# Performance work log

Hardware: AMD Instinct MI355X
Metric: run time of the kernel (lower is better)

## Reference

```python
import jax, jax.numpy as jnp
import numpy as np

NUM_HEADS = 16

def setup_inputs() -> dict:
    key = jax.random.key(0)
    ks = jax.random.split(key, 8)
    B, S, X, D = 2, 2048, 1, 1024
    scale = 1.0 / np.sqrt(D)
    return {
        "query": jax.random.normal(ks[0], (B, S, X, D), jnp.float32),
        "key": jax.random.normal(ks[1], (B, S, X, D), jnp.float32),
        "value": jax.random.normal(ks[2], (B, S, X, D), jnp.float32),
        "Wq": jax.random.normal(ks[3], (D, D), jnp.float32) * scale,
        "bq": jnp.zeros((D,), jnp.float32),
        "Wk": jax.random.normal(ks[4], (D, D), jnp.float32) * scale,
        "bk": jnp.zeros((D,), jnp.float32),
        "Wv": jax.random.normal(ks[5], (D, D), jnp.float32) * scale,
        "bv": jnp.zeros((D,), jnp.float32),
        "Wo": jax.random.normal(ks[6], (D, D), jnp.float32) * scale,
        "bo": jnp.zeros((D,), jnp.float32),
    }

def _split_heads(x, B, H):
    # [B, S, X, D] -> [B, H, S*X, depth]
    D = x.shape[-1]
    return x.reshape(B, -1, H, D // H).transpose(0, 2, 1, 3)

def reference(query, key, value, Wq, bq, Wk, bk, Wv, bv, Wo, bo):
    B, S, X, D = query.shape
    H = NUM_HEADS
    q = _split_heads(query @ Wq + bq, B, H)   # [B,H,L,dh], L=S*X
    k = _split_heads(key @ Wk + bk, B, H)
    v = _split_heads(value @ Wv + bv, B, H)
    dh = k.shape[-1]
    logits = jnp.einsum("bhqd,bhkd->bhqk", q, k) / jnp.sqrt(jnp.float32(dh))
    attn = jax.nn.softmax(logits, axis=-1)
    out = jnp.einsum("bhqk,bhkd->bhqd", attn, v)   # [B,H,L,dh]
    out = out.transpose(0, 2, 1, 3).reshape(B, S, -1, D)  # [B,S,X,D]
    return out @ Wo + bo
```

## Files before the change

kernel.cpp:

```cpp
#include <hip/hip_runtime.h>
#include <cstdint>
#include <cstddef>

typedef __bf16 bf16x8 __attribute__((ext_vector_type(8)));
typedef float f32x4 __attribute__((ext_vector_type(4)));
typedef float f32x16 __attribute__((ext_vector_type(16)));
typedef unsigned short u16;
typedef unsigned int u32;

static constexpr int Bn = 2;
static constexpr int L  = 2048;
static constexpr int Dm = 1024;
static constexpr int H  = 16;
static constexpr int DH = 64;
static constexpr int M  = Bn * L;
static constexpr size_t PER = (size_t)Bn * H * L * DH;
static constexpr int NQ = Bn * H * L;

#define SC 0.18033688f

__device__ __forceinline__ u16 f2bf(float f) {
    union { float f; u32 u; } v; v.f = f;
    u32 u = v.u + 0x7FFFu + ((v.u >> 16) & 1u);
    return (u16)(u >> 16);
}

__device__ __forceinline__ u32 pk_bf16(float a, float b) {
#if __has_builtin(__builtin_amdgcn_cvt_pk_bf16_f32)
    typedef __bf16 bf16x2_t __attribute__((ext_vector_type(2)));
    bf16x2_t t = __builtin_amdgcn_cvt_pk_bf16_f32(a, b);
    u32 r; __builtin_memcpy(&r, &t, 4); return r;
#else
    return (u32)f2bf(a) | ((u32)f2bf(b) << 16);
#endif
}
__device__ __forceinline__ u16 f2bf1(float f) { return (u16)(pk_bf16(f, f) & 0xffffu); }

__device__ __forceinline__ void gl2lds16(const void* g, void* l) {
    __builtin_amdgcn_global_load_lds(
        (const __attribute__((address_space(1))) u32*)(uintptr_t)g,
        (__attribute__((address_space(3))) u32*)(uintptr_t)l, 16, 0, 0);
}

__global__ __launch_bounds__(256) void convert_in(
    const float* __restrict__ q, const float* __restrict__ k, const float* __restrict__ v,
    u16* __restrict__ dst)
{
    const float* src = (blockIdx.y == 0) ? q : (blockIdx.y == 1) ? k : v;
    u16* d = dst + (size_t)blockIdx.y * M * Dm;
    const size_t t = (size_t)blockIdx.x * 256 + threadIdx.x;
    const float4* s4 = reinterpret_cast<const float4*>(src) + t * 2;
    float4 f0 = s4[0], f1 = s4[1];
    u32 o[4] = { pk_bf16(f0.x, f0.y), pk_bf16(f0.z, f0.w),
                 pk_bf16(f1.x, f1.y), pk_bf16(f1.z, f1.w) };
    reinterpret_cast<uint4*>(d)[t] = *reinterpret_cast<uint4*>(o);
}

__global__ __launch_bounds__(256) void convert_wt(
    const float* __restrict__ Wq, const float* __restrict__ Wk,
    const float* __restrict__ Wv, const float* __restrict__ Wo,
    u16* __restrict__ dst)
{
    __shared__ u16 Ts[64][72];
    const int z = blockIdx.z;
    const float* W = (z == 0) ? Wq : (z == 1) ? Wk : (z == 2) ? Wv : Wo;
    u16* o = dst + (size_t)z * Dm * Dm;
    const int n0 = blockIdx.x * 64, k0 = blockIdx.y * 64;
    const int tid = threadIdx.x;

    {
        const int kr = tid >> 2, nc = (tid & 3) * 16;
        const float* s = W + (size_t)(k0 + kr) * Dm + n0 + nc;
        const float4* s4 = reinterpret_cast<const float4*>(s);
        float4 a = s4[0], b = s4[1], c = s4[2], d = s4[3];
        u32 t[8] = { pk_bf16(a.x, a.y), pk_bf16(a.z, a.w), pk_bf16(b.x, b.y), pk_bf16(b.z, b.w),
                     pk_bf16(c.x, c.y), pk_bf16(c.z, c.w), pk_bf16(d.x, d.y), pk_bf16(d.z, d.w) };
        *reinterpret_cast<uint4*>(&Ts[kr][nc])     = reinterpret_cast<uint4*>(t)[0];
        *reinterpret_cast<uint4*>(&Ts[kr][nc + 8]) = reinterpret_cast<uint4*>(t)[1];
    }
    __syncthreads();
    {
        const int nr = tid >> 2, kc = (tid & 3) * 16;
        u16 w[16];
        #pragma unroll
        for (int j = 0; j < 16; ++j) w[j] = Ts[kc + j][nr];
        u16* dptr = o + (size_t)(n0 + nr) * Dm + k0 + kc;
        *reinterpret_cast<uint4*>(dptr)     = reinterpret_cast<uint4*>(w)[0];
        *reinterpret_cast<uint4*>(dptr + 8) = reinterpret_cast<uint4*>(w)[1];
    }
}

__global__ __launch_bounds__(256) void gemm_qkv(
    const u16* __restrict__ Abuf, const u16* __restrict__ Wtb,
    const float* __restrict__ bq, const float* __restrict__ bk, const float* __restrict__ bv,
    u16* __restrict__ Qh, u16* __restrict__ Kh, u16* __restrict__ Vth)
{
    __shared__ __align__(16) char smem[36864];

    const int tid = threadIdx.x;
    const int wave = tid >> 6, lane = tid & 63;
    const int quad = lane >> 4, l16 = lane & 15;
    const int wr = wave >> 1, wc = wave & 1;
    const int z = blockIdx.z;
    const u16* A  = Abuf + (size_t)z * M * Dm;
    const u16* Bt = Wtb  + (size_t)z * Dm * Dm;
    const float* bias = (z == 0) ? bq : (z == 1) ? bk : bv;
    u16* out = (z == 0) ? Qh : (z == 1) ? Kh : Vth;

    const int bid = blockIdx.y * 8 + blockIdx.x;
    const int m_idx = 4 * (bid & 7) + ((bid >> 3) & 3);
    const int n_idx = bid >> 5;
    const int n0 = n_idx * 128, m0 = m_idx * 128;

    const int srow = lane >> 2;
    const int skc  = (lane & 3) * 8;

    f32x4 acc[4][4] = {};

    auto stage = [&](int k0, int bi) {
        #pragma unroll
        for (int i = 0; i < 2; ++i) {
            const int ra = i * 64 + wave * 16;
            gl2lds16(A  + (size_t)(m0 + ra + srow) * Dm + k0 + skc, smem + bi * 8192 + ra * 64);
            gl2lds16(Bt + (size_t)(n0 + ra + srow) * Dm + k0 + skc, smem + 16384 + bi * 8192 + ra * 64);
        }
    };

    stage(0, 0);
    for (int k0 = 0, it = 0; k0 < Dm; k0 += 32, ++it) {
        const int cb = it & 1;
        __syncthreads();
        if (k0 + 32 < Dm) stage(k0 + 32, cb ^ 1);
        const u16* Asb = (const u16*)(smem + cb * 8192);
        const u16* Bsb = (const u16*)(smem + 16384 + cb * 8192);
        bf16x8 af[4], bf[4];
        #pragma unroll
        for (int t = 0; t < 4; ++t) {
            af[t] = *reinterpret_cast<const bf16x8*>(&Asb[(wr * 64 + t * 16 + l16) * 32 + quad * 8]);
            bf[t] = *reinterpret_cast<const bf16x8*>(&Bsb[(wc * 64 + t * 16 + l16) * 32 + quad * 8]);
        }
        #pragma unroll
        for (int mt = 0; mt < 4; ++mt)
            #pragma unroll
            for (int nt = 0; nt < 4; ++nt)
                acc[mt][nt] = __builtin_amdgcn_mfma_f32_16x16x32_bf16(af[mt], bf[nt], acc[mt][nt], 0, 0, 0);
    }

    __syncthreads();
    u16* tile = (u16*)smem + wave * 4608;
    const float qscale = (z == 0) ? SC : 1.0f;
    #pragma unroll
    for (int nt = 0; nt < 4; ++nt) {
        const int n = n0 + wc * 64 + nt * 16 + l16;
        const float badd = bias[n];
        const int cc = nt * 16 + l16;
        #pragma unroll
        for (int mt = 0; mt < 4; ++mt) {
            #pragma unroll
            for (int r = 0; r < 4; ++r) {
                const int rr = mt * 16 + quad * 4 + r;
                const u16 vv = f2bf1((acc[mt][nt][r] + badd) * qscale);
                if (z == 2) tile[cc * 72 + rr] = vv;
                else        tile[rr * 72 + cc] = vv;
            }
        }
    }
    __syncthreads();

    const int rsub = lane >> 3;
    const int csub = (lane & 7) * 8;
    const int h2 = (n0 + wc * 64) >> 6;
    const int mb = m0 + wr * 64;
    const int bb = mb >> 11, ll0 = mb & 2047;
    if (z == 2) {
        const size_t baseV = ((size_t)(bb * H + h2)) * DH * L;
        #pragma unroll
        for (int j = 0; j < 8; ++j) {
            const int d = j * 8 + rsub;
            uint4 vv = *reinterpret_cast<const uint4*>(&tile[d * 72 + csub]);
            *reinterpret_cast<uint4*>(out + baseV + (size_t)d * L + ll0 + csub) = vv;
        }
    } else {
        const size_t base = ((size_t)(bb * H + h2)) * L * DH;
        #pragma unroll
        for (int j = 0; j < 8; ++j) {
            const int row = j * 8 + rsub;
            uint4 vv = *reinterpret_cast<const uint4*>(&tile[row * 72 + csub]);
            *reinterpret_cast<uint4*>(out + base + (size_t)(ll0 + row) * DH + csub) = vv;
        }
    }
}

__global__ __launch_bounds__(256) void attn(
    const u16* __restrict__ Qh, const u16* __restrict__ Kh,
    const u16* __restrict__ Vth, u16* __restrict__ Opart, float* __restrict__ rsums)
{
    __shared__ __align__(16) char smem[32768];
    u16* Os = (u16*)smem;

    const int tid  = threadIdx.x;
    const int wave = tid >> 6, lane = tid & 63;
    const int l31  = lane & 31, hh = lane >> 5;
    const int qt = blockIdx.x >> 1, half = blockIdx.x & 1;
    const int h = blockIdx.y, b = blockIdx.z;
    const size_t hb = ((size_t)(b * H + h)) * L * DH;
    const int q0 = qt * 128 + wave * 32;

    u16*  Op = Opart + (size_t)half * PER;
    float* rp = rsums + (size_t)half * NQ;

    bf16x8 qf[4];
    {
        const u16* qp = Qh + hb + (size_t)(q0 + l31) * DH + hh * 8;
        #pragma unroll
        for (int c = 0; c < 4; ++c)
            qf[c] = *reinterpret_cast<const bf16x8*>(qp + c * 16);
    }

    bf16x8 ones;
    {
        u32 ov[4] = { 0x3F803F80u, 0x3F803F80u, 0x3F803F80u, 0x3F803F80u };
        ones = *reinterpret_cast<bf16x8*>(ov);
    }

    const int r_off = lane >> 3;
    const int s_sl  = lane & 7;

    auto stage = [&](int kt, int bi) {
        char* base = smem + bi * 16384;
        #pragma unroll
        for (int i = 0; i < 2; ++i) {
            const int rr = wave * 16 + i * 8 + r_off;
            gl2lds16(Kh  + hb + (size_t)(kt * 64 + rr) * DH + ((s_sl ^ (rr & 7)) << 3),
                     base + (wave * 16 + i * 8) * 128);
            gl2lds16(Vth + hb + (size_t)rr * L + kt * 64 + ((s_sl ^ (rr & 7)) << 3),
                     base + 8192 + (wave * 16 + i * 8) * 128);
        }
    };

    int vbK[2], vbV[2];
    #pragma unroll
    for (int t = 0; t < 2; ++t) {
        const int rr = t * 32 + l31;
        vbK[t] = rr * 128 + ((rr & 7) << 4);
        vbV[t] = 8192 + rr * 128 + ((rr & 7) << 4);
    }

    f32x16 oacc[2] = {};
    f32x16 oaccR = {};

    const int kt0 = half * 16;
    stage(kt0, 0);
    for (int ktl = 0; ktl < 16; ++ktl) {
        const int cb = ktl & 1;
        __syncthreads();
        if (ktl + 1 < 16) stage(kt0 + ktl + 1, cb ^ 1);
        const char* ldsb = smem + cb * 16384;

        f32x16 st[2] = {};
        #pragma unroll
        for (int t = 0; t < 2; ++t) {
            #pragma unroll
            for (int c = 0; c < 4; ++c) {
                bf16x8 kf = *reinterpret_cast<const bf16x8*>(ldsb + (vbK[t] ^ (((c << 1) | hh) << 4)));
                st[t] = __builtin_amdgcn_mfma_f32_32x32x16_bf16(kf, qf[c], st[t], 0, 0, 0);
            }
        }

        bf16x8 pfrag[4];
        #pragma unroll
        for (int t = 0; t < 2; ++t) {
            float p[16];
            #pragma unroll
            for (int rr = 0; rr < 16; ++rr)
                p[rr] = __builtin_amdgcn_exp2f(st[t][rr]);
            #pragma unroll
            for (int g = 0; g < 2; ++g) {
                float* pg = p + g * 8;
                u32 w0 = pk_bf16(pg[0], pg[1]);
                u32 w1 = pk_bf16(pg[2], pg[3]);
                u32 w2 = pk_bf16(pg[4], pg[5]);
                u32 w3 = pk_bf16(pg[6], pg[7]);
                asm volatile("v_permlane32_swap_b32 %0, %1" : "+v"(w0), "+v"(w2));
                asm volatile("v_permlane32_swap_b32 %0, %1" : "+v"(w1), "+v"(w3));
                u32 pkv[4] = { w0, w1, w2, w3 };
                pfrag[t * 2 + g] = *reinterpret_cast<bf16x8*>(pkv);
            }
        }

        #pragma unroll
        for (int c = 0; c < 4; ++c) {
            #pragma unroll
            for (int t = 0; t < 2; ++t) {
                bf16x8 vf = *reinterpret_cast<const bf16x8*>(ldsb + (vbV[t] ^ (((c << 1) | hh) << 4)));
                oacc[t] = __builtin_amdgcn_mfma_f32_32x32x16_bf16(vf, pfrag[c], oacc[t], 0, 0, 0);
            }
            oaccR = __builtin_amdgcn_mfma_f32_32x32x16_bf16(ones, pfrag[c], oaccR, 0, 0, 0);
        }
    }

    #pragma unroll
    for (int pass = 0; pass < 2; ++pass) {
        __syncthreads();
        if ((wave >> 1) == pass) {
            const int qloc = (wave & 1) * 32 + l31;
            #pragma unroll
            for (int t = 0; t < 2; ++t) {
                #pragma unroll
                for (int rq = 0; rq < 4; ++rq) {
                    const int d0 = t * 32 + rq * 8 + hh * 4;
                    *reinterpret_cast<u32*>(&Os[qloc * 72 + d0]) =
                        pk_bf16(oacc[t][rq * 4 + 0], oacc[t][rq * 4 + 1]);
                    *reinterpret_cast<u32*>(&Os[qloc * 72 + d0 + 2]) =
                        pk_bf16(oacc[t][rq * 4 + 2], oacc[t][rq * 4 + 3]);
                }
            }
        }
        __syncthreads();
        {
            const int row = tid >> 2, cc = (tid & 3) * 16;
            u16* dst = Op + hb + (size_t)(qt * 128 + pass * 64 + row) * DH + cc;
            *reinterpret_cast<uint4*>(dst)     = *reinterpret_cast<const uint4*>(&Os[row * 72 + cc]);
            *reinterpret_cast<uint4*>(dst + 8) = *reinterpret_cast<const uint4*>(&Os[row * 72 + cc + 8]);
        }
    }
    if (hh == 0) rp[((size_t)(b * H + h)) * L + q0 + l31] = oaccR[0];
}

__global__ __launch_bounds__(256) void attn_merge(
    const u16* __restrict__ O0, const u16* __restrict__ O1,
    const float* __restrict__ r0, const float* __restrict__ r1,
    u16* __restrict__ ctx)
{
    const int g = blockIdx.x * 256 + threadIdx.x;
    const int row = g >> 3, dc = (g & 7) * 8;
    const int b = row >> 15, h = (row >> 11) & (H - 1), l = row & (L - 1);
    const float inv = 1.0f / (r0[row] + r1[row]);
    bf16x8 a = *reinterpret_cast<const bf16x8*>(O0 + (size_t)row * DH + dc);
    bf16x8 c = *reinterpret_cast<const bf16x8*>(O1 + (size_t)row * DH + dc);
    u32 o[4];
    #pragma unroll
    for (int i = 0; i < 4; ++i)
        o[i] = pk_bf16(((float)a[2 * i] + (float)c[2 * i]) * inv,
                       ((float)a[2 * i + 1] + (float)c[2 * i + 1]) * inv);
    *reinterpret_cast<uint4*>(ctx + ((size_t)(b * L + l)) * Dm + h * DH + dc) =
        *reinterpret_cast<uint4*>(o);
}

__global__ __launch_bounds__(512) void gemm_out(
    const u16* __restrict__ A, const u16* __restrict__ Bt,
    const float* __restrict__ bias, float* __restrict__ out)
{
    __shared__ u16 As[2][128 * 32];
    __shared__ u16 Bs[2][128 * 32];
    const int tid = threadIdx.x;
    const int wave = tid >> 6, lane = tid & 63;
    const int quad = lane >> 4, l16 = lane & 15;
    const int wr = wave >> 1, wc = wave & 1;
    const int n0 = blockIdx.x * 128, m0 = blockIdx.y * 128;

    const int srow = lane >> 2;
    const int skc  = (lane & 3) * 8;

    f32x4 acc[2][4] = {};

    auto stage = [&](int k0, int bi) {
        gl2lds16(A  + (size_t)(m0 + wave * 16 + srow) * Dm + k0 + skc, &As[bi][(wave * 16) * 32]);
        gl2lds16(Bt + (size_t)(n0 + wave * 16 + srow) * Dm + k0 + skc, &Bs[bi][(wave * 16) * 32]);
    };

    stage(0, 0);
    for (int k0 = 0, it = 0; k0 < Dm; k0 += 32, ++it) {
        const int cb = it & 1;
        __syncthreads();
        if (k0 + 32 < Dm) stage(k0 + 32, cb ^ 1);
        bf16x8 af[2], bf[4];
        #pragma unroll
        for (int t = 0; t < 2; ++t)
            af[t] = *reinterpret_cast<const bf16x8*>(&As[cb][(wr * 32 + t * 16 + l16) * 32 + quad * 8]);
        #pragma unroll
        for (int t = 0; t < 4; ++t)
            bf[t] = *reinterpret_cast<const bf16x8*>(&Bs[cb][(wc * 64 + t * 16 + l16) * 32 + quad * 8]);
        #pragma unroll
        for (int mt = 0; mt < 2; ++mt)
            #pragma unroll
            for (int nt = 0; nt < 4; ++nt)
                acc[mt][nt] = __builtin_amdgcn_mfma_f32_16x16x32_bf16(af[mt], bf[nt], acc[mt][nt], 0, 0, 0);
    }

    #pragma unroll
    for (int nt = 0; nt < 4; ++nt) {
        const int n = n0 + wc * 64 + nt * 16 + l16;
        const float badd = bias[n];
        #pragma unroll
        for (int mt = 0; mt < 2; ++mt) {
            #pragma unroll
            for (int r = 0; r < 4; ++r) {
                const int m = m0 + wr * 32 + mt * 16 + quad * 4 + r;
                out[(size_t)m * Dm + n] = acc[mt][nt][r] + badd;
            }
        }
    }
}

extern "C" void kernel_launch(void* const* d_in, const int* in_sizes, int n_in,
                              void* d_out, int out_size, void* d_ws, size_t ws_size,
                              hipStream_t stream) {
    const float* q  = (const float*)d_in[0];
    const float* k  = (const float*)d_in[1];
    const float* v  = (const float*)d_in[2];
    const float* Wq = (const float*)d_in[3];
    const float* bq = (const float*)d_in[4];
    const float* Wk = (const float*)d_in[5];
    const float* bk = (const float*)d_in[6];
    const float* Wv = (const float*)d_in[7];
    const float* bv = (const float*)d_in[8];
    const float* Wo = (const float*)d_in[9];
    const float* bo = (const float*)d_in[10];
    float* out = (float*)d_out;

    u16* Abuf = (u16*)d_ws;
    u16* Wt   = Abuf + 3 * (size_t)M * Dm;
    u16* Qh   = Wt + 4 * (size_t)Dm * Dm;
    u16* Kh   = Qh + PER;
    u16* Vth  = Kh + PER;
    u16* O0   = Vth + PER;
    float* rs = (float*)(O0 + 2 * PER);
    u16* ctx  = Abuf;

    convert_in <<<dim3((M * Dm) / 8 / 256, 3), 256, 0, stream>>>(q, k, v, Abuf);
    convert_wt <<<dim3(Dm / 64, Dm / 64, 4), 256, 0, stream>>>(Wq, Wk, Wv, Wo, Wt);
    gemm_qkv   <<<dim3(Dm / 128, M / 128, 3), 256, 0, stream>>>(Abuf, Wt, bq, bk, bv, Qh, Kh, Vth);
    attn       <<<dim3(L / 128 * 2, H, Bn), 256, 0, stream>>>(Qh, Kh, Vth, O0, rs);
    attn_merge <<<NQ * 8 / 256, 256, 0, stream>>>(O0, O0 + PER, rs, rs + NQ, ctx);
    gemm_out   <<<dim3(Dm / 128, M / 128), 512, 0, stream>>>(ctx, Wt + 3 * (size_t)Dm * Dm, bo, out);
}
```

Measured before the change: 235.8 us.

## Load K/V fragments directly from global and accumulate softmax row sums in registers

Drops the double-buffered global-to-LDS staging of K and V tiles and the per-tile block barriers. Each wave now reads its K and V MFMA fragments straight from global memory. The row-sum MFMA against a ones vector is replaced by a per-lane fp32 sum of the exponentials, combined across half-waves with a shuffle. This removes LDS traffic, barriers and one MFMA per step. The cost is that all four waves fetch the same K/V data separately, and the global loads are no longer prefetched a tile ahead, which may expose memory latency.

Result: slower. 296.8 us (+25.9%).

```diff
diff --git a/kernel.cpp b/kernel.cpp
--- a/kernel.cpp
+++ b/kernel.cpp
@@ -195,8 +195,7 @@
     const u16* __restrict__ Qh, const u16* __restrict__ Kh,
     const u16* __restrict__ Vth, u16* __restrict__ Opart, float* __restrict__ rsums)
 {
-    __shared__ __align__(16) char smem[32768];
-    u16* Os = (u16*)smem;
+    __shared__ u16 Os[64 * 72];
 
     const int tid  = threadIdx.x;
     const int wave = tid >> 6, lane = tid & 63;
@@ -217,54 +216,23 @@
             qf[c] = *reinterpret_cast<const bf16x8*>(qp + c * 16);
     }
 
-    bf16x8 ones;
-    {
-        u32 ov[4] = { 0x3F803F80u, 0x3F803F80u, 0x3F803F80u, 0x3F803F80u };
-        ones = *reinterpret_cast<bf16x8*>(ov);
-    }
-
-    const int r_off = lane >> 3;
-    const int s_sl  = lane & 7;
-
-    auto stage = [&](int kt, int bi) {
-        char* base = smem + bi * 16384;
-        #pragma unroll
-        for (int i = 0; i < 2; ++i) {
-            const int rr = wave * 16 + i * 8 + r_off;
-            gl2lds16(Kh  + hb + (size_t)(kt * 64 + rr) * DH + ((s_sl ^ (rr & 7)) << 3),
-                     base + (wave * 16 + i * 8) * 128);
-            gl2lds16(Vth + hb + (size_t)rr * L + kt * 64 + ((s_sl ^ (rr & 7)) << 3),
-                     base + 8192 + (wave * 16 + i * 8) * 128);
-        }
-    };
-
-    int vbK[2], vbV[2];
-    #pragma unroll
-    for (int t = 0; t < 2; ++t) {
-        const int rr = t * 32 + l31;
-        vbK[t] = rr * 128 + ((rr & 7) << 4);
-        vbV[t] = 8192 + rr * 128 + ((rr & 7) << 4);
-    }
-
+    const int kt0 = half * 16;
+    const u16* kp0 = Kh  + hb + (size_t)(kt0 * 64 + l31) * DH + hh * 8;
+    const u16* kp1 = kp0 + 32 * DH;
+    const u16* vp0 = Vth + hb + (size_t)l31 * L + kt0 * 64 + hh * 8;
+    const u16* vp1 = vp0 + (size_t)32 * L;
+
+    float rsum = 0.f;
     f32x16 oacc[2] = {};
-    f32x16 oaccR = {};
-
-    const int kt0 = half * 16;
-    stage(kt0, 0);
+
     for (int ktl = 0; ktl < 16; ++ktl) {
-        const int cb = ktl & 1;
-        __syncthreads();
-        if (ktl + 1 < 16) stage(kt0 + ktl + 1, cb ^ 1);
-        const char* ldsb = smem + cb * 16384;
-
         f32x16 st[2] = {};
         #pragma unroll
-        for (int t = 0; t < 2; ++t) {
-            #pragma unroll
-            for (int c = 0; c < 4; ++c) {
-                bf16x8 kf = *reinterpret_cast<const bf16x8*>(ldsb + (vbK[t] ^ (((c << 1) | hh) << 4)));
-                st[t] = __builtin_amdgcn_mfma_f32_32x32x16_bf16(kf, qf[c], st[t], 0, 0, 0);
-            }
+        for (int c = 0; c < 4; ++c) {
+            bf16x8 k0 = *reinterpret_cast<const bf16x8*>(kp0 + c * 16);
+            bf16x8 k1 = *reinterpret_cast<const bf16x8*>(kp1 + c * 16);
+            st[0] = __builtin_amdgcn_mfma_f32_32x32x16_bf16(k0, qf[c], st[0], 0, 0, 0);
+            st[1] = __builtin_amdgcn_mfma_f32_32x32x16_bf16(k1, qf[c], st[1], 0, 0, 0);
         }
 
         bf16x8 pfrag[4];
@@ -272,8 +240,10 @@
         for (int t = 0; t < 2; ++t) {
             float p[16];
             #pragma unroll
-            for (int rr = 0; rr < 16; ++rr)
+            for (int rr = 0; rr < 16; ++rr) {
                 p[rr] = __builtin_amdgcn_exp2f(st[t][rr]);
+                rsum += p[rr];
+            }
             #pragma unroll
             for (int g = 0; g < 2; ++g) {
                 float* pg = p + g * 8;
@@ -290,14 +260,17 @@
 
         #pragma unroll
         for (int c = 0; c < 4; ++c) {
-            #pragma unroll
-            for (int t = 0; t < 2; ++t) {
-                bf16x8 vf = *reinterpret_cast<const bf16x8*>(ldsb + (vbV[t] ^ (((c << 1) | hh) << 4)));
-                oacc[t] = __builtin_amdgcn_mfma_f32_32x32x16_bf16(vf, pfrag[c], oacc[t], 0, 0, 0);
-            }
-            oaccR = __builtin_amdgcn_mfma_f32_32x32x16_bf16(ones, pfrag[c], oaccR, 0, 0, 0);
-        }
-    }
+            bf16x8 v0 = *reinterpret_cast<const bf16x8*>(vp0 + c * 16);
+            bf16x8 v1 = *reinterpret_cast<const bf16x8*>(vp1 + c * 16);
+            oacc[0] = __builtin_amdgcn_mfma_f32_32x32x16_bf16(v0, pfrag[c], oacc[0], 0, 0, 0);
+            oacc[1] = __builtin_amdgcn_mfma_f32_32x32x16_bf16(v1, pfrag[c], oacc[1], 0, 0, 0);
+        }
+
+        kp0 += 64 * DH; kp1 += 64 * DH;
+        vp0 += 64;      vp1 += 64;
+    }
+
+    rsum += __shfl_xor(rsum, 32);
 
     #pragma unroll
     for (int pass = 0; pass < 2; ++pass) {
@@ -324,7 +297,7 @@
             *reinterpret_cast<uint4*>(dst + 8) = *reinterpret_cast<const uint4*>(&Os[row * 72 + cc + 8]);
         }
     }
-    if (hh == 0) rp[((size_t)(b * H + h)) * L + q0 + l31] = oaccR[0];
+    if (hh == 0) rp[((size_t)(b * H + h)) * L + q0 + l31] = rsum;
 }
 
 __global__ __launch_bounds__(256) void attn_merge(
```
